# Performance work log

Hardware: AMD Instinct MI355X
Metric: run time of the kernel (lower is better)

The kernel has to match this reference:

```python
import jax, jax.numpy as jnp
import numpy as np

U = 8          # units per modular layer
B = 16384      # batch
IN = 512       # input feature dim
H = 512        # modular hidden dim
NC = 62        # n_class


def _aggregate(P, h):
    # P: [T, F] policy link matrix; h: [F, B, D] per-unit features.
    # agg[t] = sum_f P[t,f] * h[f], normalized by row-sum when row-sum > 0.
    s = jnp.einsum('tf,fbd->tbd', P, h)
    row = P.sum(axis=1)                      # [T]
    safe = jnp.where(row > 0, row, 1.0)[:, None, None]
    return jnp.where((row > 0)[:, None, None], s / safe, s)


def setup_inputs() -> dict:
    key = jax.random.key(0)
    ks = jax.random.split(key, 12)
    s_in = 1.0 / np.sqrt(IN)
    s_h = 1.0 / np.sqrt(H)
    return {
        'x': jax.random.normal(ks[0], (B, IN), jnp.float32),
        'policy1': jax.random.uniform(ks[1], (U * U,), jnp.float32),
        'policy2': jax.random.uniform(ks[2], (U * U,), jnp.float32),
        'policy_final': jax.random.uniform(ks[3], (U,), jnp.float32),
        'W0': jax.random.uniform(ks[4], (U, IN, H), jnp.float32, -s_in, s_in),
        'b0': jax.random.uniform(ks[5], (U, H), jnp.float32, -s_in, s_in),
        'W1': jax.random.uniform(ks[6], (U, H, H), jnp.float32, -s_h, s_h),
        'b1': jax.random.uniform(ks[7], (U, H), jnp.float32, -s_h, s_h),
        'W2': jax.random.uniform(ks[8], (U, H, NC), jnp.float32, -s_h, s_h),
        'b2': jax.random.uniform(ks[9], (U, NC), jnp.float32, -s_h, s_h),
    }


def reference(x, policy1, policy2, policy_final, W0, b0, W1, b1, W2, b2):
    # Layer 0 (input modular layer): policy_list[0] is forced to all-ones,
    # so every unit sees x unscaled. Each unit: Linear + ReLU.
    h0 = jax.nn.relu(jnp.einsum('bi,uid->ubd', x, W0) + b0[:, None, :])  # [U,B,H]

    # Mid layer: policy-gated weighted-sum aggregation, then per-unit Linear+ReLU.
    a1 = _aggregate(policy1.reshape(U, U), h0)
    h1 = jax.nn.relu(jnp.einsum('ubi,uid->ubd', a1, W1) + b1[:, None, :])

    # Output modular layer: aggregate then per-unit Linear (no activation).
    a2 = _aggregate(policy2.reshape(U, U), h1)
    h2 = jnp.einsum('ubi,uic->ubc', a2, W2) + b2[:, None, :]  # [U,B,NC]

    # Final gating. Original code divides by divider INSIDE the unit loop
    # (every iteration), so replicate that recurrence exactly.
    d = policy_final.sum()
    inv = jnp.where(d > 0, 1.0 / jnp.where(d > 0, d, 1.0), 1.0)
    out = jnp.zeros((B, NC), jnp.float32)
    for j in range(U):  # fixed small unit count, not a data dim
        out = (out + h2[j] * policy_final[j]) * inv
    return out
```

## Files before the change

kernel.cpp:

```cpp
#include <hip/hip_runtime.h>

#define U_   8
#define B_   16384
#define NC_  62

typedef __attribute__((ext_vector_type(8))) short bfrag;
typedef __attribute__((ext_vector_type(4))) float facc;

__device__ __forceinline__ float bf2f(unsigned int lo16) {
    union { unsigned int i; float f; } v;
    v.i = lo16 << 16;
    return v.f;
}
__device__ __forceinline__ unsigned short f2bf(float f) {
    unsigned int x = __float_as_uint(f);
    return (unsigned short)((x + 0x7fffu + ((x >> 16) & 1u)) >> 16);
}
__device__ __forceinline__ void gl2lds16(const void* g, void* l) {
    __builtin_amdgcn_global_load_lds(
        (const __attribute__((address_space(1))) void*)g,
        (__attribute__((address_space(3))) void*)l, 16, 0, 0);
}
__device__ __forceinline__ void cfence() { asm volatile("" ::: "memory"); }
__device__ __forceinline__ void bar() {
    asm volatile("" ::: "memory");
    __builtin_amdgcn_s_barrier();
    asm volatile("" ::: "memory");
}
__device__ __forceinline__ void barL() {
    asm volatile("s_waitcnt lgkmcnt(0)" ::: "memory");
    __builtin_amdgcn_s_barrier();
    asm volatile("" ::: "memory");
}
#define VMCNT(n) asm volatile("s_waitcnt vmcnt(" #n ")" ::: "memory")

__global__ __launch_bounds__(256) void prep_all(
    const float* __restrict__ p2, const float* __restrict__ pf,
    const float* __restrict__ W0, const float* __restrict__ W1,
    const float* __restrict__ W2, const float* __restrict__ x,
    unsigned short* __restrict__ W0r, unsigned short* __restrict__ W1t,
    unsigned short* __restrict__ Woutt, unsigned short* __restrict__ xb)
{
    __shared__ float tile[32][33];
    const int b = blockIdx.x;

    if (b < 4096) {
        const bool isW0 = (b < 2048);
        const int bb = isW0 ? b : b - 2048;
        const int u  = bb >> 8;
        const int n0 = (bb & 15) * 32, k0 = ((bb >> 4) & 15) * 32;
        const int tx = threadIdx.x & 31, ty = threadIdx.x >> 5;
        const float* Wb = (isW0 ? W0 : W1) + (long)u * 512 * 512;
#pragma unroll
        for (int i = 0; i < 4; i++)
            tile[ty + i * 8][tx] = Wb[(long)(k0 + ty + i * 8) * 512 + n0 + tx];
        __syncthreads();
        if (isW0) {
#pragma unroll
            for (int i = 0; i < 4; i++) {
                int n = n0 + ty + i * 8, k = k0 + tx;
                int np = (n >> 5) * 256 + u * 32 + (n & 31);
                W0r[(long)np * 512 + k] = f2bf(tile[tx][ty + i * 8]);
            }
        } else {
            unsigned short* Wo = W1t + (long)u * 512 * 512;
#pragma unroll
            for (int i = 0; i < 4; i++) {
                int n = n0 + ty + i * 8, k = k0 + tx;
                Wo[(long)n * 512 + k] = f2bf(tile[tx][ty + i * 8]);
            }
        }
    } else if (b < 5120) {
        const int bx = b - 4096;
        const int c   = threadIdx.x & 63;
        const int row = bx * 4 + (threadIdx.x >> 6);
        const int f = row >> 9, k = row & 511;
        float d = 0.f;
#pragma unroll
        for (int j = 0; j < 8; j++) d += pf[j];
        float inv = d > 0.f ? 1.f / d : 1.f;
        float s = 0.f;
        if (c < NC_) {
#pragma unroll
            for (int u = 0; u < 8; u++) {
                float wv = pf[u];
#pragma unroll
                for (int i = u; i < 8; i++) wv *= inv;
                float s2 = 0.f;
#pragma unroll
                for (int ff = 0; ff < 8; ff++) s2 += p2[u * 8 + ff];
                float p2n = p2[u * 8 + f] * (s2 > 0.f ? 1.f / s2 : 1.f);
                s += wv * p2n * W2[((long)u * 512 + k) * NC_ + c];
            }
        }
        Woutt[(long)c * 4096 + row] = f2bf(s);
    } else {
        const int bx = b - 5120;
        long i = ((long)bx * 256 + threadIdx.x) * 8;
        if (i >= (long)B_ * 512) return;
        const float4* xp = (const float4*)(x + i);
        float4 a = xp[0], bb4 = xp[1];
        uint4 o;
        o.x = f2bf(a.x) | ((unsigned)f2bf(a.y) << 16);
        o.y = f2bf(a.z) | ((unsigned)f2bf(a.w) << 16);
        o.z = f2bf(bb4.x) | ((unsigned)f2bf(bb4.y) << 16);
        o.w = f2bf(bb4.z) | ((unsigned)f2bf(bb4.w) << 16);
        *(uint4*)(xb + i) = o;
    }
}

__global__ __launch_bounds__(256, 2) void gemm0_mix(
    const unsigned short* __restrict__ xb, const unsigned short* __restrict__ W0r,
    const float* __restrict__ b0, const float* __restrict__ p1,
    unsigned short* __restrict__ a1, long plane)
{
    __shared__ __align__(16) unsigned short sm[33792];
    const int tid = threadIdx.x, w = tid >> 6, lane = tid & 63;
    const int flat = blockIdx.x;
    const int xcd = flat & 7, seq = flat >> 3;
    const int ng = xcd * 2 + (seq & 1);
    const long mBase = (long)(seq >> 1) * 128;

    const int lr = lane >> 2;
    const int lg = (lane & 3) ^ ((lane >> 3) & 3);
    const int wm = w >> 1, wn = w & 1;
    const int r = lane & 15, q = lane >> 4;
    const int xq = (q ^ ((r >> 1) & 3)) * 8;

    facc acc[4][8];
#pragma unroll
    for (int i = 0; i < 4; i++)
#pragma unroll
        for (int j = 0; j < 8; j++) acc[i][j] = (facc){0.f, 0.f, 0.f, 0.f};

    auto stage = [&](int buf, int kt) {
        const int k0 = kt * 32;
        unsigned short* dA = sm + buf * 4096;
        unsigned short* dB = sm + 8192 + buf * 8192;
#pragma unroll
        for (int i = 0; i < 2; i++) {
            const int c = w * 2 + i;
            gl2lds16(xb + (mBase + c * 16 + lr) * 512 + k0 + lg * 8, dA + c * 512);
        }
#pragma unroll
        for (int i = 0; i < 4; i++) {
            const int c = w * 4 + i;
            gl2lds16(W0r + ((long)ng * 256 + c * 16 + lr) * 512 + k0 + lg * 8,
                     dB + c * 512);
        }
    };
    auto compute = [&](int buf) {
        const unsigned short* sA = sm + buf * 4096;
        const unsigned short* sB = sm + 8192 + buf * 8192;
        bfrag aF[4], bF[8];
#pragma unroll
        for (int mt = 0; mt < 4; mt++)
            aF[mt] = *(const bfrag*)&sA[(wm * 64 + mt * 16 + r) * 32 + xq];
#pragma unroll
        for (int nt = 0; nt < 8; nt++)
            bF[nt] = *(const bfrag*)&sB[(wn * 128 + nt * 16 + r) * 32 + xq];
#pragma unroll
        for (int mt = 0; mt < 4; mt++)
#pragma unroll
            for (int nt = 0; nt < 8; nt++)
                acc[mt][nt] = __builtin_amdgcn_mfma_f32_16x16x32_bf16(
                    aF[mt], bF[nt], acc[mt][nt], 0, 0, 0);
    };

    stage(0, 0);
    cfence();
    stage(1, 1);
    VMCNT(6);
    bar();
#pragma unroll
    for (int t = 0; t < 16; ++t) {
        compute(t & 1);
        if (t <= 13) {
            barL();
            stage(t & 1, t + 2);
            VMCNT(6);
            bar();
        } else if (t == 14) {
            VMCNT(0);
            bar();
        } else {
            barL();
        }
    }

#pragma unroll
    for (int nt = 0; nt < 8; nt++) {
        const int cl = wn * 128 + nt * 16 + r;
        const float bv = b0[(cl >> 5) * 512 + ng * 32 + (cl & 31)];
#pragma unroll
        for (int mt = 0; mt < 4; mt++) {
            const int rowb = wm * 64 + mt * 16 + q * 4;
#pragma unroll
            for (int rg = 0; rg < 4; rg++) {
                float v = acc[mt][nt][rg] + bv;
                v = v > 0.f ? v : 0.f;
                sm[(rowb + rg) * 264 + cl] = f2bf(v);
            }
        }
    }
    __syncthreads();

    float pw[64];
#pragma unroll
    for (int t8 = 0; t8 < 8; t8++) {
        float s1 = 0.f;
#pragma unroll
        for (int f = 0; f < 8; f++) s1 += p1[t8 * 8 + f];
        float inv = s1 > 0.f ? 1.f / s1 : 1.f;
#pragma unroll
        for (int f = 0; f < 8; f++) pw[t8 * 8 + f] = p1[t8 * 8 + f] * inv;
    }
    const int row = tid >> 1, fs0 = (tid & 1) * 16;
    float hv[8][16];
#pragma unroll
    for (int u = 0; u < 8; u++) {
        bfrag ha = *(const bfrag*)&sm[row * 264 + u * 32 + fs0];
        bfrag hb = *(const bfrag*)&sm[row * 264 + u * 32 + fs0 + 8];
#pragma unroll
        for (int j = 0; j < 8; j++) {
            hv[u][j]     = bf2f((unsigned int)(unsigned short)ha[j]);
            hv[u][j + 8] = bf2f((unsigned int)(unsigned short)hb[j]);
        }
    }
    const long rowOff = (mBase + row) * 512 + ng * 32 + fs0;
#pragma unroll
    for (int t = 0; t < 8; t++) {
        float o[16];
#pragma unroll
        for (int j = 0; j < 16; j++) {
            float s = 0.f;
#pragma unroll
            for (int u = 0; u < 8; u++) s = fmaf(pw[t * 8 + u], hv[u][j], s);
            o[j] = s;
        }
        uint4 ov0, ov1;
        ov0.x = f2bf(o[0])  | ((unsigned)f2bf(o[1])  << 16);
        ov0.y = f2bf(o[2])  | ((unsigned)f2bf(o[3])  << 16);
        ov0.z = f2bf(o[4])  | ((unsigned)f2bf(o[5])  << 16);
        ov0.w = f2bf(o[6])  | ((unsigned)f2bf(o[7])  << 16);
        ov1.x = f2bf(o[8])  | ((unsigned)f2bf(o[9])  << 16);
        ov1.y = f2bf(o[10]) | ((unsigned)f2bf(o[11]) << 16);
        ov1.z = f2bf(o[12]) | ((unsigned)f2bf(o[13]) << 16);
        ov1.w = f2bf(o[14]) | ((unsigned)f2bf(o[15]) << 16);
        *(uint4*)(a1 + (long)t * plane + rowOff)     = ov0;
        *(uint4*)(a1 + (long)t * plane + rowOff + 8) = ov1;
    }
}

__global__ __launch_bounds__(256, 2) void gemm_hout(
    const unsigned short* __restrict__ a1,
    const unsigned short* __restrict__ W1t,
    const float* __restrict__ b1,
    const unsigned short* __restrict__ Woutt,
    float* __restrict__ partial, long plane)
{
    __shared__ __align__(16) unsigned short sm[36864];
    const int tid = threadIdx.x, w = tid >> 6, lane = tid & 63;
    const int flat = blockIdx.x;
    const int u = flat & 7, seq = flat >> 3;
    const long mBase = (long)seq * 64;
    const long Bc = plane >> 9;

    const int lr = lane >> 2;
    const int lg = (lane & 3) ^ ((lane >> 3) & 3);
    const int r = lane & 15, q = lane >> 4;
    const int xq = (q ^ ((r >> 1) & 3)) * 8;

    const unsigned short* Ab = a1 + (long)u * plane;
    const unsigned short* Bb = W1t + (long)u * 512 * 512;

    const unsigned short* WgL =
        Woutt + (long)(w * 16 + r) * 4096 + u * 512 + q * 8;
    bfrag bW[16];
#pragma unroll
    for (int kt = 0; kt < 16; ++kt)
        bW[kt] = *(const bfrag*)(WgL + kt * 32);

    facc acc[4][8];
#pragma unroll
    for (int i = 0; i < 4; i++)
#pragma unroll
        for (int j = 0; j < 8; j++) acc[i][j] = (facc){0.f, 0.f, 0.f, 0.f};

    auto stage = [&](int buf, int kt) {
        const int k0 = kt * 32;
        unsigned short* dA = sm + buf * 2048;
        unsigned short* dB = sm + 4096 + buf * 16384;
        gl2lds16(Ab + (mBase + w * 16 + lr) * 512 + k0 + lg * 8, dA + w * 512);
#pragma unroll
        for (int i = 0; i < 8; i++) {
            const int c = w * 8 + i;
            gl2lds16(Bb + (long)(c * 16 + lr) * 512 + k0 + lg * 8, dB + c * 512);
        }
    };
    auto compute = [&](int buf) {
        const unsigned short* sA = sm + buf * 2048;
        const unsigned short* sB = sm + 4096 + buf * 16384;
        bfrag aF[4], bF[8];
#pragma unroll
        for (int mt = 0; mt < 4; mt++)
            aF[mt] = *(const bfrag*)&sA[(mt * 16 + r) * 32 + xq];
#pragma unroll
        for (int nt = 0; nt < 8; nt++)
            bF[nt] = *(const bfrag*)&sB[(w * 128 + nt * 16 + r) * 32 + xq];
#pragma unroll
        for (int mt = 0; mt < 4; mt++)
#pragma unroll
            for (int nt = 0; nt < 8; nt++)
                acc[mt][nt] = __builtin_amdgcn_mfma_f32_16x16x32_bf16(
                    aF[mt], bF[nt], acc[mt][nt], 0, 0, 0);
    };

    stage(0, 0);
    cfence();
    stage(1, 1);
    VMCNT(9);
    bar();
#pragma unroll
    for (int t = 0; t < 16; ++t) {
        compute(t & 1);
        if (t <= 13) {
            barL();
            stage(t & 1, t + 2);
            VMCNT(9);
            bar();
        } else if (t == 14) {
            VMCNT(0);
            bar();
        } else {
            barL();
        }
    }

#pragma unroll
    for (int nt = 0; nt < 8; nt++) {
        const int col = w * 128 + nt * 16 + r;
        const float bv = b1[u * 512 + col];
#pragma unroll
        for (int mt = 0; mt < 4; mt++) {
            const int rowb = mt * 16 + q * 4;
#pragma unroll
            for (int rg = 0; rg < 4; rg++) {
                float v = acc[mt][nt][rg] + bv;
                v = v > 0.f ? v : 0.f;
                sm[(rowb + rg) * 522 + col] = f2bf(v);
            }
        }
    }
    __syncthreads();

    facc acc2[4];
#pragma unroll
    for (int i = 0; i < 4; i++) acc2[i] = (facc){0.f, 0.f, 0.f, 0.f};
#pragma unroll
    for (int kt = 0; kt < 16; ++kt) {
#pragma unroll
        for (int mt = 0; mt < 4; mt++) {
            bfrag aH = *(const bfrag*)&sm[(mt * 16 + r) * 522 + kt * 32 + q * 8];
            acc2[mt] = __builtin_amdgcn_mfma_f32_16x16x32_bf16(
                aH, bW[kt], acc2[mt], 0, 0, 0);
        }
    }

    float* pb = partial + ((long)u * Bc + mBase) * 64;
#pragma unroll
    for (int mt = 0; mt < 4; mt++) {
#pragma unroll
        for (int rg = 0; rg < 4; rg++) {
            const int prow = mt * 16 + q * 4 + rg;
            pb[(long)prow * 64 + w * 16 + r] = acc2[mt][rg];
        }
    }
}

__global__ __launch_bounds__(256) void reduce_out(
    const float* __restrict__ partial, const float* __restrict__ pf,
    const float* __restrict__ b2, float* __restrict__ out, int Bc)
{
    const long flat = (long)blockIdx.x * 256 + threadIdx.x;
    const long row = flat >> 2;
    const int cg = (int)(flat & 3) * 16;
    float s[16];
#pragma unroll
    for (int j = 0; j < 16; j++) s[j] = 0.f;
#pragma unroll
    for (int u = 0; u < 8; u++) {
        const float4* p = (const float4*)(partial + ((long)u * Bc + row) * 64 + cg);
#pragma unroll
        for (int v4 = 0; v4 < 4; v4++) {
            float4 v = p[v4];
            s[v4 * 4 + 0] += v.x; s[v4 * 4 + 1] += v.y;
            s[v4 * 4 + 2] += v.z; s[v4 * 4 + 3] += v.w;
        }
    }
    float d = 0.f;
#pragma unroll
    for (int j = 0; j < 8; j++) d += pf[j];
    float inv = d > 0.f ? 1.f / d : 1.f;
    float wv[8];
#pragma unroll
    for (int j = 0; j < 8; j++) {
        float v = pf[j];
#pragma unroll
        for (int i = j; i < 8; i++) v *= inv;
        wv[j] = v;
    }
#pragma unroll
    for (int j = 0; j < 16; j++) {
        const int c = cg + j;
        if (c < NC_) {
            float cc = 0.f;
#pragma unroll
            for (int u = 0; u < 8; u++) cc += wv[u] * b2[u * NC_ + c];
            out[row * NC_ + c] = s[j] + cc;
        }
    }
}

extern "C" void kernel_launch(void* const* d_in, const int* in_sizes, int n_in,
                              void* d_out, int out_size, void* d_ws, size_t ws_size,
                              hipStream_t stream)
{
    const float* x  = (const float*)d_in[0];
    const float* p1 = (const float*)d_in[1];
    const float* p2 = (const float*)d_in[2];
    const float* pf = (const float*)d_in[3];
    const float* W0 = (const float*)d_in[4];
    const float* b0 = (const float*)d_in[5];
    const float* W1 = (const float*)d_in[6];
    const float* b1 = (const float*)d_in[7];
    const float* W2 = (const float*)d_in[8];
    const float* b2 = (const float*)d_in[9];
    float* out = (float*)d_out;

    char* ws = (char*)d_ws;
    size_t off = 0;
    auto alloc = [&](size_t bytes) -> void* {
        void* p = ws + off;
        off += (bytes + 255) & ~(size_t)255;
        return p;
    };
    unsigned short* W0r   = (unsigned short*)alloc((size_t)4096 * 512 * 2);
    unsigned short* W1t   = (unsigned short*)alloc((size_t)U_ * 512 * 512 * 2);
    unsigned short* Woutt = (unsigned short*)alloc((size_t)64 * 4096 * 2);
    unsigned short* xb    = (unsigned short*)alloc((size_t)B_ * 512 * 2);

    size_t remain = ws_size > off ? ws_size - off : 0;
    int Bc = 2048;
    for (int cand = B_; cand >= 2048; cand >>= 1) {
        size_t need = 8ull * cand * 512 * 2 + 8ull * cand * 64 * 4 + 1024;
        if (need <= remain) { Bc = cand; break; }
    }
    unsigned short* a1 = (unsigned short*)alloc(8ull * Bc * 512 * 2);
    float* partial     = (float*)alloc(8ull * Bc * 64 * 4);

    prep_all<<<dim3(9216), 256, 0, stream>>>(
        p2, pf, W0, W1, W2, x, W0r, W1t, Woutt, xb);

    const int Mb = Bc / 128;
    const long plane = (long)Bc * 512;
    for (int bb = 0; bb < B_; bb += Bc) {
        gemm0_mix<<<dim3(16 * Mb), 256, 0, stream>>>(
            xb + (long)bb * 512, W0r, b0, p1, a1, plane);
        gemm_hout<<<dim3(8 * (Bc / 64)), 256, 0, stream>>>(
            a1, W1t, b1, Woutt, partial, plane);
        reduce_out<<<dim3(Bc / 64), 256, 0, stream>>>(
            partial, pf, b2, out + (long)bb * NC_, Bc);
    }
}
```

Baseline: 344.9 us.

## Split output projection into separate K=4096 GEMM instead of per-unit partials plus reduce

The per-unit output projection and fp32 partial buffer are removed from the hidden-layer GEMM kernel, which now writes bf16 h1 to global memory. A new gemm_out kernel runs one GEMM over the concatenated unit dimension (K=4096, N=64) with double-buffered LDS staging, and applies the folded bias and gating in its epilogue. This replaces the separate reduce kernel and frees registers held by the preloaded output weights in the hidden GEMM. In exchange it writes and rereads a full bf16 h1 buffer, and gemm_out launches only Bc/64 blocks, which may leave the GPU underused.

New measurement: 360.3 us. 1.04x slower.

```diff
diff --git a/kernel.cpp b/kernel.cpp
--- a/kernel.cpp
+++ b/kernel.cpp
@@ -252,19 +252,17 @@
     }
 }
 
-__global__ __launch_bounds__(256, 2) void gemm_hout(
+__global__ __launch_bounds__(256, 2) void gemm_h(
     const unsigned short* __restrict__ a1,
     const unsigned short* __restrict__ W1t,
     const float* __restrict__ b1,
-    const unsigned short* __restrict__ Woutt,
-    float* __restrict__ partial, long plane)
+    unsigned short* __restrict__ h1, long plane)
 {
     __shared__ __align__(16) unsigned short sm[36864];
     const int tid = threadIdx.x, w = tid >> 6, lane = tid & 63;
     const int flat = blockIdx.x;
     const int u = flat & 7, seq = flat >> 3;
     const long mBase = (long)seq * 64;
-    const long Bc = plane >> 9;
 
     const int lr = lane >> 2;
     const int lg = (lane & 3) ^ ((lane >> 3) & 3);
@@ -273,13 +271,6 @@
 
     const unsigned short* Ab = a1 + (long)u * plane;
     const unsigned short* Bb = W1t + (long)u * 512 * 512;
-
-    const unsigned short* WgL =
-        Woutt + (long)(w * 16 + r) * 4096 + u * 512 + q * 8;
-    bfrag bW[16];
-#pragma unroll
-    for (int kt = 0; kt < 16; ++kt)
-        bW[kt] = *(const bfrag*)(WgL + kt * 32);
 
     facc acc[4][8];
 #pragma unroll
@@ -348,56 +339,97 @@
             for (int rg = 0; rg < 4; rg++) {
                 float v = acc[mt][nt][rg] + bv;
                 v = v > 0.f ? v : 0.f;
-                sm[(rowb + rg) * 522 + col] = f2bf(v);
+                sm[(rowb + rg) * 520 + col] = f2bf(v);
             }
         }
     }
     __syncthreads();
 
-    facc acc2[4];
-#pragma unroll
-    for (int i = 0; i < 4; i++) acc2[i] = (facc){0.f, 0.f, 0.f, 0.f};
-#pragma unroll
-    for (int kt = 0; kt < 16; ++kt) {
-#pragma unroll
-        for (int mt = 0; mt < 4; mt++) {
-            bfrag aH = *(const bfrag*)&sm[(mt * 16 + r) * 522 + kt * 32 + q * 8];
-            acc2[mt] = __builtin_amdgcn_mfma_f32_16x16x32_bf16(
-                aH, bW[kt], acc2[mt], 0, 0, 0);
-        }
-    }
-
-    float* pb = partial + ((long)u * Bc + mBase) * 64;
-#pragma unroll
-    for (int mt = 0; mt < 4; mt++) {
-#pragma unroll
-        for (int rg = 0; rg < 4; rg++) {
-            const int prow = mt * 16 + q * 4 + rg;
-            pb[(long)prow * 64 + w * 16 + r] = acc2[mt][rg];
-        }
-    }
-}
-
-__global__ __launch_bounds__(256) void reduce_out(
-    const float* __restrict__ partial, const float* __restrict__ pf,
-    const float* __restrict__ b2, float* __restrict__ out, int Bc)
+    unsigned short* Cb = h1 + (long)u * plane + mBase * 512;
+#pragma unroll
+    for (int it = 0; it < 16; it++) {
+        const int g = tid + it * 256;
+        const int row = g >> 6, gr = g & 63;
+        *(uint4*)(Cb + (long)row * 512 + gr * 8) = *(const uint4*)&sm[row * 520 + gr * 8];
+    }
+}
+
+__global__ __launch_bounds__(256, 1) void gemm_out(
+    const unsigned short* __restrict__ h1,
+    const unsigned short* __restrict__ Bt,
+    const float* __restrict__ pf, const float* __restrict__ b2,
+    float* __restrict__ out, long plane)
 {
-    const long flat = (long)blockIdx.x * 256 + threadIdx.x;
-    const long row = flat >> 2;
-    const int cg = (int)(flat & 3) * 16;
-    float s[16];
-#pragma unroll
-    for (int j = 0; j < 16; j++) s[j] = 0.f;
-#pragma unroll
-    for (int u = 0; u < 8; u++) {
-        const float4* p = (const float4*)(partial + ((long)u * Bc + row) * 64 + cg);
-#pragma unroll
-        for (int v4 = 0; v4 < 4; v4++) {
-            float4 v = p[v4];
-            s[v4 * 4 + 0] += v.x; s[v4 * 4 + 1] += v.y;
-            s[v4 * 4 + 2] += v.z; s[v4 * 4 + 3] += v.w;
-        }
-    }
+    __shared__ __align__(16) unsigned short sm[16384];
+    const int tid = threadIdx.x, w = tid >> 6, lane = tid & 63;
+    const long mBase = (long)blockIdx.x * 64;
+
+    const int lr = lane >> 3, lg = (lane & 7) ^ lr;
+    const int wm = w >> 1, wn = w & 1;
+    const int r = lane & 15, q = lane >> 4;
+    const int x7 = r & 7;
+
+    facc acc[2][2];
+#pragma unroll
+    for (int i = 0; i < 2; i++)
+#pragma unroll
+        for (int j = 0; j < 2; j++) acc[i][j] = (facc){0.f, 0.f, 0.f, 0.f};
+
+    auto stage = [&](int buf, int it) {
+        const int u = it >> 3;
+        const int kk = (it & 7) * 64;
+        unsigned short* dA = sm + buf * 4096;
+        unsigned short* dB = sm + 8192 + buf * 4096;
+#pragma unroll
+        for (int i = 0; i < 2; i++) {
+            const int c = w * 2 + i;
+            gl2lds16(h1 + (long)u * plane + (mBase + c * 8 + lr) * 512 + kk + lg * 8,
+                     dA + c * 512);
+            gl2lds16(Bt + (long)(c * 8 + lr) * 4096 + u * 512 + kk + lg * 8,
+                     dB + c * 512);
+        }
+    };
+    auto compute = [&](int buf) {
+        const unsigned short* sA = sm + buf * 4096;
+        const unsigned short* sB = sm + 8192 + buf * 4096;
+#pragma unroll
+        for (int h = 0; h < 2; h++) {
+            const int xg = ((h * 4 + q) ^ x7) * 8;
+            bfrag aF[2], bF[2];
+#pragma unroll
+            for (int mt = 0; mt < 2; mt++)
+                aF[mt] = *(const bfrag*)&sA[(wm * 32 + mt * 16 + r) * 64 + xg];
+#pragma unroll
+            for (int nt = 0; nt < 2; nt++)
+                bF[nt] = *(const bfrag*)&sB[(wn * 32 + nt * 16 + r) * 64 + xg];
+#pragma unroll
+            for (int mt = 0; mt < 2; mt++)
+#pragma unroll
+                for (int nt = 0; nt < 2; nt++)
+                    acc[mt][nt] = __builtin_amdgcn_mfma_f32_16x16x32_bf16(
+                        aF[mt], bF[nt], acc[mt][nt], 0, 0, 0);
+        }
+    };
+
+    stage(0, 0);
+    cfence();
+    stage(1, 1);
+    VMCNT(4);
+    bar();
+#pragma unroll 2
+    for (int t = 0; t < 64; ++t) {
+        compute(t & 1);
+        if (t <= 61) {
+            barL();
+            stage(t & 1, t + 2);
+            VMCNT(4);
+            bar();
+        } else if (t == 62) {
+            VMCNT(0);
+            bar();
+        }
+    }
+
     float d = 0.f;
 #pragma unroll
     for (int j = 0; j < 8; j++) d += pf[j];
@@ -411,13 +443,21 @@
         wv[j] = v;
     }
 #pragma unroll
-    for (int j = 0; j < 16; j++) {
-        const int c = cg + j;
-        if (c < NC_) {
-            float cc = 0.f;
-#pragma unroll
-            for (int u = 0; u < 8; u++) cc += wv[u] * b2[u * NC_ + c];
-            out[row * NC_ + c] = s[j] + cc;
+    for (int nt = 0; nt < 2; nt++) {
+        const int col = wn * 32 + nt * 16 + r;
+        float cc = 0.f;
+        if (col < NC_) {
+#pragma unroll
+            for (int u = 0; u < 8; u++) cc += wv[u] * b2[u * NC_ + col];
+        }
+#pragma unroll
+        for (int mt = 0; mt < 2; mt++) {
+#pragma unroll
+            for (int rg = 0; rg < 4; rg++) {
+                const int row = wm * 32 + mt * 16 + q * 4 + rg;
+                if (col < NC_)
+                    out[(mBase + row) * NC_ + col] = acc[mt][nt][rg] + cc;
+            }
         }
     }
 }
@@ -453,11 +493,11 @@
     size_t remain = ws_size > off ? ws_size - off : 0;
     int Bc = 2048;
     for (int cand = B_; cand >= 2048; cand >>= 1) {
-        size_t need = 8ull * cand * 512 * 2 + 8ull * cand * 64 * 4 + 1024;
+        size_t need = 2ull * 8 * cand * 512 * 2 + 1024;
         if (need <= remain) { Bc = cand; break; }
     }
     unsigned short* a1 = (unsigned short*)alloc(8ull * Bc * 512 * 2);
-    float* partial     = (float*)alloc(8ull * Bc * 64 * 4);
+    unsigned short* h1 = (unsigned short*)alloc(8ull * Bc * 512 * 2);
 
     prep_all<<<dim3(9216), 256, 0, stream>>>(
         p2, pf, W0, W1, W2, x, W0r, W1t, Woutt, xb);
@@ -467,9 +507,8 @@
     for (int bb = 0; bb < B_; bb += Bc) {
         gemm0_mix<<<dim3(16 * Mb), 256, 0, stream>>>(
             xb + (long)bb * 512, W0r, b0, p1, a1, plane);
-        gemm_hout<<<dim3(8 * (Bc / 64)), 256, 0, stream>>>(
-            a1, W1t, b1, Woutt, partial, plane);
-        reduce_out<<<dim3(Bc / 64), 256, 0, stream>>>(
-            partial, pf, b2, out + (long)bb * NC_, Bc);
-    }
-}
+        gemm_h<<<dim3(8 * (Bc / 64)), 256, 0, stream>>>(a1, W1t, b1, h1, plane);
+        gemm_out<<<dim3(Bc / 64), 256, 0, stream>>>(
+            h1, Woutt, pf, b2, out + (long)bb * NC_, plane);
+    }
+}
```
